# Kernel tuning notes

Hardware: AMD Instinct MI355X
Metric: run time of the kernel (lower is better)

Reference implementation:

```python
import jax, jax.numpy as jnp
import numpy as np

B, C, H, W = 32, 384, 28, 28
E, HID, K = 4, 384, 2  # HID = hidden_features(1536) // num_experts(4)


def setup_inputs() -> dict:
    key = jax.random.key(0)
    ks = jax.random.split(key, 5)
    x = jax.random.normal(ks[0], (B, C, H, W), jnp.float32)
    gate_w = jax.random.normal(ks[1], (C, E), jnp.float32) * 0.02
    gate_b = jnp.zeros((E,), jnp.float32)
    w1 = jax.random.normal(ks[2], (E, HID, C), jnp.float32) * 0.02
    b1 = jnp.zeros((E, HID), jnp.float32)
    w2 = jax.random.normal(ks[3], (E, C, HID), jnp.float32) * 0.02
    b2 = jnp.zeros((E, C), jnp.float32)
    return {"x": x, "gate_w": gate_w, "gate_b": gate_b,
            "w1": w1, "b1": b1, "w2": w2, "b2": b2}


def reference(x, gate_w, gate_b, w1, b1, w2, b2):
    b, c, h, w = x.shape
    e = gate_b.shape[0]
    # per-token gating: tokens are spatial positions in NHWC order
    x_flat = x.transpose(0, 2, 3, 1).reshape(-1, c)          # [N, C], N = B*H*W
    scores = jax.nn.softmax(x_flat @ gate_w + gate_b, -1)    # [N, E]
    top_v, top_i = jax.lax.top_k(scores, K)                  # [N, K]
    top_w = jax.nn.softmax(top_v, -1)                        # [N, K] renormalized
    # weight map per top-k slot: [K, B, H, W]
    wmap = top_w.T.reshape(K, b, h, w)
    # faithful to torch loop: expert i contributes at slot k iff ANY token routed
    # to it at slot k; the weight applied is the UNMASKED slot-k weight map.
    present = (top_i[:, :, None] == jnp.arange(e)[None, None, :]).any(0)  # [K, E]
    coef = jnp.einsum('ke,kbhw->ebhw', present.astype(x.dtype), wmap)     # [E, B, H, W]
    # dense per-expert 1x1-conv MLP over the FULL tensor (as in the source)
    hdn = jax.nn.relu(jnp.einsum('bchw,edc->ebdhw', x, w1)
                      + b1[:, None, :, None, None])          # [E, B, HID, H, W]
    y = jnp.einsum('ebdhw,eod->ebohw', hdn, w2) + b2[:, None, :, None, None]
    out = jnp.einsum('ebohw,ebhw->bohw', y, coef)            # [B, C, H, W]
    return out
```

## Files before the change

### kernel.cpp

```cpp
#include <hip/hip_runtime.h>
#include <hip/hip_bf16.h>
#include <stdint.h>

#define B_DIM 32
#define C_DIM 384
#define HW_DIM 784
#define E_DIM 4
#define HID_DIM 384
#define NTOK (B_DIM * HW_DIM)
#define NH (E_DIM * HID_DIM)

using short8 = __attribute__((ext_vector_type(8))) short;
using f32x4  = __attribute__((ext_vector_type(4))) float;
typedef unsigned short ushort_t;

__device__ __forceinline__ ushort_t f2bf(float f) {
  __hip_bfloat16 h = __float2bfloat16(f);
  return __builtin_bit_cast(ushort_t, h);
}

__device__ __forceinline__ void gload_lds16(const void* g, void* l) {
  __builtin_amdgcn_global_load_lds(
      (const __attribute__((address_space(1))) unsigned int*)g,
      (__attribute__((address_space(3))) unsigned int*)l, 16, 0, 0);
}

__global__ __launch_bounds__(256) void prep_kernel(
    const float* __restrict__ w1, const float* __restrict__ w2,
    ushort_t* __restrict__ W1b, ushort_t* __restrict__ W2b,
    unsigned int* __restrict__ present) {
  int i = blockIdx.x * 256 + threadIdx.x;
  if (i == 0) *present = 0u;
  if (i < NH * C_DIM) {
    W1b[i] = f2bf(w1[i]);
    int o = i / NH;
    int r = i - o * NH;
    int e = r / HID_DIM;
    int k = r - e * HID_DIM;
    W2b[i] = f2bf(w2[((size_t)e * C_DIM + o) * HID_DIM + k]);
  }
}

__global__ __launch_bounds__(512) void gate_kernel(
    const float* __restrict__ x, const float* __restrict__ gw,
    const float* __restrict__ gb, ushort_t* __restrict__ xb,
    float* __restrict__ topw, unsigned int* __restrict__ present) {
  __shared__ __align__(16) ushort_t lxs[64][392];
  __shared__ float pscore[8][64][4];
  __shared__ unsigned int pmask;
  const int b = blockIdx.x;
  const int p0 = blockIdx.y * 64;
  const int cnt = min(64, HW_DIM - p0);
  const int tid = threadIdx.x;
  const int cg = tid >> 6, tl = tid & 63;
  if (tid == 0) pmask = 0u;
  float a0 = 0.f, a1 = 0.f, a2 = 0.f, a3 = 0.f;
  const bool valid = tl < cnt;
  if (valid) {
    const float* xp = x + (size_t)b * C_DIM * HW_DIM + p0 + tl;
    for (int c = cg; c < C_DIM; c += 8) {
      const float v = xp[(size_t)c * HW_DIM];
      lxs[tl][c] = f2bf(v);
      const float4 g = *(const float4*)&gw[c * 4];
      a0 += v * g.x; a1 += v * g.y; a2 += v * g.z; a3 += v * g.w;
    }
  }
  pscore[cg][tl][0] = a0; pscore[cg][tl][1] = a1;
  pscore[cg][tl][2] = a2; pscore[cg][tl][3] = a3;
  __syncthreads();
  if (cg == 0 && valid) {
    float z[4];
#pragma unroll
    for (int e = 0; e < 4; e++) {
      float s = gb[e];
#pragma unroll
      for (int g8 = 0; g8 < 8; g8++) s += pscore[g8][tl][e];
      z[e] = s;
    }
    const float mx = fmaxf(fmaxf(z[0], z[1]), fmaxf(z[2], z[3]));
    float s[4]; float sum = 0.f;
#pragma unroll
    for (int e = 0; e < 4; e++) { s[e] = __expf(z[e] - mx); sum += s[e]; }
    const float inv = 1.f / sum;
#pragma unroll
    for (int e = 0; e < 4; e++) s[e] *= inv;
    int e0 = 0; float v0 = s[0];
#pragma unroll
    for (int e = 1; e < 4; e++) if (s[e] > v0) { v0 = s[e]; e0 = e; }
    int e1 = -1; float v1 = -1.f;
#pragma unroll
    for (int e = 0; e < 4; e++) if (e != e0 && s[e] > v1) { v1 = s[e]; e1 = e; }
    const float r = __expf(v1 - v0);
    const float w0 = 1.f / (1.f + r);
    const int m = b * HW_DIM + p0 + tl;
    topw[m * 2] = w0;
    topw[m * 2 + 1] = 1.f - w0;
    atomicOr(&pmask, (1u << e0) | (1u << (4 + e1)));
  }
  __syncthreads();
  if (tid == 0) atomicOr(present, pmask);
  const int nchunk = cnt * 48;
  for (int ci = tid; ci < nchunk; ci += 512) {
    const int row = ci / 48, c8 = ci - row * 48;
    short8 v = *(const short8*)&lxs[row][c8 * 8];
    *(short8*)&xb[(size_t)(b * HW_DIM + p0 + row) * C_DIM + c8 * 8] = v;
  }
}

__global__ __launch_bounds__(256, 3) void gemm_1b(
    const ushort_t* __restrict__ A, const ushort_t* __restrict__ Bw,
    const float* __restrict__ bias, const float* __restrict__ topw,
    const unsigned int* __restrict__ presentp, ushort_t* __restrict__ hOut) {
  constexpr int KDIM = C_DIM, BM = 128, BN = 128, BK = 32;
  constexpr int KT = KDIM / BK;
  constexpr int NTN = NH / BN;
  constexpr int ASZ = BM * BK;
  __shared__ ushort_t smem[6 * ASZ];

  const int nwg = NTN * (NTOK / BM);
  const int orig = blockIdx.x;
  const int xcd = orig & 7;
  const int qq = nwg >> 3, rr = nwg & 7;
  const int wg = (xcd < rr ? xcd * (qq + 1) : rr * (qq + 1) + (xcd - rr) * qq)
               + (orig >> 3);
  const int mt = wg / NTN, nt = wg % NTN;
  const int m0 = mt * BM, n0 = nt * BN;

  const int tid = threadIdx.x;
  const int lane = tid & 63;
  const int wid = tid >> 6;
  const int wm = wid >> 1, wn = wid & 1;
  const int lanel = lane & 15, laneq = lane >> 4;

  auto stage = [&](int t) {
    const int buf = t % 3;
    ushort_t* dstA = smem + buf * ASZ;
    ushort_t* dstB = smem + 3 * ASZ + buf * ASZ;
    const int kb = t * BK;
#pragma unroll
    for (int li = 0; li < 2; ++li) {
      const int P = (li * 256 + tid) * 16;
      const int row = P >> 6;
      const int cb = (P & 63) ^ (((row >> 1) & 3) << 4);
      gload_lds16(&A[(size_t)(m0 + row) * KDIM + kb + (cb >> 1)],
                  (char*)dstA + P);
    }
#pragma unroll
    for (int li = 0; li < 2; ++li) {
      const int P = (li * 256 + tid) * 16;
      const int row = P >> 6;
      const int cb = (P & 63) ^ (((row >> 1) & 3) << 4);
      gload_lds16(&Bw[(size_t)(n0 + row) * KDIM + kb + (cb >> 1)],
                  (char*)dstB + P);
    }
  };

  f32x4 acc[4][4] = {};
  const int cbr = (laneq * 16) ^ (((lanel >> 1) & 3) << 4);

  stage(0);
  stage(1);
  for (int t = 0; t < KT; ++t) {
    if (t + 1 < KT)
      asm volatile("s_waitcnt vmcnt(4)" ::: "memory");
    else
      asm volatile("s_waitcnt vmcnt(0)" ::: "memory");
    __builtin_amdgcn_sched_barrier(0);
    __builtin_amdgcn_s_barrier();
    __builtin_amdgcn_sched_barrier(0);
    if (t + 2 < KT) stage(t + 2);
    const int buf = t % 3;
    const char* Ab = (const char*)(smem + buf * ASZ) + (wm * 64 + lanel) * 64;
    const char* Bb =
        (const char*)(smem + 3 * ASZ + buf * ASZ) + (wn * 64 + lanel) * 64;
    short8 av[4], bv[4];
#pragma unroll
    for (int i = 0; i < 4; ++i) av[i] = *(const short8*)(Ab + i * 1024 + cbr);
#pragma unroll
    for (int j = 0; j < 4; ++j) bv[j] = *(const short8*)(Bb + j * 1024 + cbr);
    __builtin_amdgcn_s_setprio(1);
#pragma unroll
    for (int i = 0; i < 4; ++i)
#pragma unroll
      for (int j = 0; j < 4; ++j)
        acc[i][j] = __builtin_amdgcn_mfma_f32_16x16x32_bf16(
            av[i], bv[j], acc[i][j], 0, 0, 0);
    __builtin_amdgcn_s_setprio(0);
  }

  const unsigned int pm = *presentp;
  __syncthreads();
  ushort_t* tr = smem;
  const int e = n0 / HID_DIM;
  const float P0 = (float)((pm >> e) & 1u);
  const float P1 = (float)((pm >> (4 + e)) & 1u);
#pragma unroll
  for (int mi = 0; mi < 4; ++mi) {
    const int r0 = wm * 64 + mi * 16 + laneq * 4;
    const int mg = m0 + r0;
    const float4 t0 = *(const float4*)&topw[mg * 2];
    const float4 t1 = *(const float4*)&topw[mg * 2 + 4];
    const float cj[4] = {P0 * t0.x + P1 * t0.y, P0 * t0.z + P1 * t0.w,
                         P0 * t1.x + P1 * t1.y, P0 * t1.z + P1 * t1.w};
#pragma unroll
    for (int ni = 0; ni < 4; ++ni) {
      const int cl = wn * 64 + ni * 16 + lanel;
      const float bvv = bias[n0 + cl];
#pragma unroll
      for (int j = 0; j < 4; ++j) {
        float v = fmaxf(acc[mi][ni][j] + bvv, 0.f);
        tr[(r0 + j) * 128 + cl] = f2bf(cj[j] * v);
      }
    }
  }
  __syncthreads();
#pragma unroll
  for (int it = 0; it < 8; ++it) {
    const int c = it * 256 + tid;
    const int row = c >> 4, cr = c & 15;
    *(short8*)&hOut[(size_t)(m0 + row) * NH + n0 + cr * 8] =
        *(const short8*)&tr[row * 128 + cr * 8];
  }
}

__global__ __launch_bounds__(128, 2) void gemm2_t(
    const ushort_t* __restrict__ A, const ushort_t* __restrict__ Bw,
    const float* __restrict__ bias, const float* __restrict__ topw,
    const unsigned int* __restrict__ presentp, float* __restrict__ outp) {
  constexpr int KDIM = NH, BM = 64, BN = 128, BK = 32;
  constexpr int KT = KDIM / BK;
  constexpr int NTN = C_DIM / BN;
  constexpr int ASZ = BM * BK;
  constexpr int BSZ = BN * BK;
  __shared__ ushort_t smem[3 * ASZ + 2 * BSZ];

  const int nwg = NTN * (NTOK / BM);
  const int orig = blockIdx.x;
  const int xcd = orig & 7;
  const int qq = nwg >> 3, rr = nwg & 7;
  const int wg = (xcd < rr ? xcd * (qq + 1) : rr * (qq + 1) + (xcd - rr) * qq)
               + (orig >> 3);
  const int mt = wg / NTN, nt = wg % NTN;
  const int m0 = mt * BM, n0 = nt * BN;

  const int tid = threadIdx.x;
  const int lane = tid & 63;
  const int wn = tid >> 6;
  const int lanel = lane & 15, laneq = lane >> 4;

  auto stageA = [&](int t) {
    ushort_t* dst = smem + (t % 3) * ASZ;
    const int kb = t * BK;
#pragma unroll
    for (int li = 0; li < 2; ++li) {
      const int P = (li * 128 + tid) * 16;
      const int row = P >> 6;
      const int cb = (P & 63) ^ (((row >> 1) & 3) << 4);
      gload_lds16(&A[(size_t)(m0 + row) * KDIM + kb + (cb >> 1)],
                  (char*)dst + P);
    }
  };
  auto stageB = [&](int t) {
    ushort_t* dst = smem + 3 * ASZ + (t & 1) * BSZ;
    const int kb = t * BK;
#pragma unroll
    for (int li = 0; li < 4; ++li) {
      const int P = (li * 128 + tid) * 16;
      const int row = P >> 6;
      const int cb = (P & 63) ^ (((row >> 1) & 3) << 4);
      gload_lds16(&Bw[(size_t)(n0 + row) * KDIM + kb + (cb >> 1)],
                  (char*)dst + P);
    }
  };

  f32x4 acc[4][4] = {};
  const int cbr = (laneq * 16) ^ (((lanel >> 1) & 3) << 4);

  stageA(0);
  stageB(0);
  stageA(1);
  for (int t = 0; t < KT; ++t) {
    if (t + 1 < KT)
      asm volatile("s_waitcnt vmcnt(2)" ::: "memory");
    else
      asm volatile("s_waitcnt vmcnt(0)" ::: "memory");
    __builtin_amdgcn_sched_barrier(0);
    __builtin_amdgcn_s_barrier();
    __builtin_amdgcn_sched_barrier(0);
    if (t + 1 < KT) stageB(t + 1);
    if (t + 2 < KT) stageA(t + 2);
    const char* Ab = (const char*)(smem + (t % 3) * ASZ) + lanel * 64;
    const char* Bb = (const char*)(smem + 3 * ASZ + (t & 1) * BSZ) +
                     (wn * 64 + lanel) * 64;
    short8 av[4], bv[4];
#pragma unroll
    for (int i = 0; i < 4; ++i) av[i] = *(const short8*)(Ab + i * 1024 + cbr);
#pragma unroll
    for (int j = 0; j < 4; ++j) bv[j] = *(const short8*)(Bb + j * 1024 + cbr);
    __builtin_amdgcn_s_setprio(1);
#pragma unroll
    for (int i = 0; i < 4; ++i)
#pragma unroll
      for (int j = 0; j < 4; ++j)
        acc[i][j] = __builtin_amdgcn_mfma_f32_16x16x32_bf16(
            av[i], bv[j], acc[i][j], 0, 0, 0);
    __builtin_amdgcn_s_setprio(0);
  }

  const unsigned int pm = *presentp;
  float B0[4], B1[4];
#pragma unroll
  for (int ni = 0; ni < 4; ++ni) {
    const int o = n0 + wn * 64 + ni * 16 + lanel;
    float s0 = 0.f, s1 = 0.f;
#pragma unroll
    for (int e2 = 0; e2 < 4; ++e2) {
      const float bb = bias[e2 * C_DIM + o];
      s0 += (float)((pm >> e2) & 1u) * bb;
      s1 += (float)((pm >> (4 + e2)) & 1u) * bb;
    }
    B0[ni] = s0; B1[ni] = s1;
  }
#pragma unroll
  for (int mi = 0; mi < 4; ++mi) {
    const int mg = m0 + mi * 16 + laneq * 4;
    const float4 t0 = *(const float4*)&topw[mg * 2];
    const float4 t1 = *(const float4*)&topw[mg * 2 + 4];
    const int bb2 = mg / HW_DIM;
    const int p = mg - bb2 * HW_DIM;
#pragma unroll
    for (int ni = 0; ni < 4; ++ni) {
      const int o = n0 + wn * 64 + ni * 16 + lanel;
      float4 v;
      v.x = acc[mi][ni][0] + t0.x * B0[ni] + t0.y * B1[ni];
      v.y = acc[mi][ni][1] + t0.z * B0[ni] + t0.w * B1[ni];
      v.z = acc[mi][ni][2] + t1.x * B0[ni] + t1.y * B1[ni];
      v.w = acc[mi][ni][3] + t1.z * B0[ni] + t1.w * B1[ni];
      *(float4*)&outp[((size_t)bb2 * C_DIM + o) * HW_DIM + p] = v;
    }
  }
}

extern "C" void kernel_launch(void* const* d_in, const int* in_sizes, int n_in,
                              void* d_out, int out_size, void* d_ws, size_t ws_size,
                              hipStream_t stream) {
  const float* x  = (const float*)d_in[0];
  const float* gw = (const float*)d_in[1];
  const float* gb = (const float*)d_in[2];
  const float* w1 = (const float*)d_in[3];
  const float* b1 = (const float*)d_in[4];
  const float* w2 = (const float*)d_in[5];
  const float* b2 = (const float*)d_in[6];
  float* out = (float*)d_out;

  char* ws = (char*)d_ws;
  ushort_t* xb = (ushort_t*)ws;   ws += (size_t)NTOK * C_DIM * 2;
  ushort_t* hdnS = (ushort_t*)ws; ws += (size_t)NTOK * NH * 2;
  ushort_t* W1b = (ushort_t*)ws;  ws += (size_t)NH * C_DIM * 2;
  ushort_t* W2b = (ushort_t*)ws;  ws += (size_t)C_DIM * NH * 2;
  float* topw = (float*)ws;       ws += (size_t)NTOK * 2 * 4;
  unsigned int* present = (unsigned int*)ws;

  prep_kernel<<<dim3((NH * C_DIM) / 256), dim3(256), 0, stream>>>(
      w1, w2, W1b, W2b, present);
  gate_kernel<<<dim3(B_DIM, 13), dim3(512), 0, stream>>>(
      x, gw, gb, xb, topw, present);
  gemm_1b<<<dim3((NTOK / 128) * (NH / 128)), dim3(256), 0, stream>>>(
      xb, W1b, b1, topw, present, hdnS);
  gemm2_t<<<dim3((NTOK / 64) * (C_DIM / 128)), dim3(128), 0, stream>>>(
      hdnS, W2b, b2, topw, present, out);
}
```

Baseline: 131.2 us.

## Swap GEMM tile configs: 2-wave 128x128 for GEMM1, 4-wave 128x128 for GEMM2

GEMM1 moves from 4 waves with 64x64 warp tiles to 2 waves, each computing a 128x64 tile with 32 accumulators, double-buffered with a full vmcnt(0) wait each step. GEMM2 now reuses the former 4-wave 128x128 pipeline with a 128-row M tile instead of 64, which halves how often the B operand is reloaded per output. Larger per-wave tiles raise MFMA-to-LDS-load ratio but increase register pressure and reduce latency hiding from the simpler pipeline.

Result: no change. 128.7 us (-1.9%).

```diff
diff --git a/kernel.cpp b/kernel.cpp
--- a/kernel.cpp
+++ b/kernel.cpp
@@ -107,13 +107,122 @@
   }
 }
 
-__global__ __launch_bounds__(256, 3) void gemm_1b(
+__global__ __launch_bounds__(128, 2) void gemm_w2(
     const ushort_t* __restrict__ A, const ushort_t* __restrict__ Bw,
     const float* __restrict__ bias, const float* __restrict__ topw,
     const unsigned int* __restrict__ presentp, ushort_t* __restrict__ hOut) {
   constexpr int KDIM = C_DIM, BM = 128, BN = 128, BK = 32;
   constexpr int KT = KDIM / BK;
   constexpr int NTN = NH / BN;
+  constexpr int ASZ = BM * BK;
+  __shared__ ushort_t smem[4 * ASZ];
+
+  const int nwg = NTN * (NTOK / BM);
+  const int orig = blockIdx.x;
+  const int xcd = orig & 7;
+  const int qq = nwg >> 3, rr = nwg & 7;
+  const int wg = (xcd < rr ? xcd * (qq + 1) : rr * (qq + 1) + (xcd - rr) * qq)
+               + (orig >> 3);
+  const int mt = wg / NTN, nt = wg % NTN;
+  const int m0 = mt * BM, n0 = nt * BN;
+
+  const int tid = threadIdx.x;
+  const int lane = tid & 63;
+  const int wn = tid >> 6;
+  const int lanel = lane & 15, laneq = lane >> 4;
+
+  auto stage = [&](int t) {
+    ushort_t* dstA = smem + (t & 1) * ASZ;
+    ushort_t* dstB = smem + 2 * ASZ + (t & 1) * ASZ;
+    const int kb = t * BK;
+#pragma unroll
+    for (int li = 0; li < 4; ++li) {
+      const int P = (li * 128 + tid) * 16;
+      const int row = P >> 6;
+      const int cb = (P & 63) ^ (((row >> 1) & 3) << 4);
+      gload_lds16(&A[(size_t)(m0 + row) * KDIM + kb + (cb >> 1)],
+                  (char*)dstA + P);
+    }
+#pragma unroll
+    for (int li = 0; li < 4; ++li) {
+      const int P = (li * 128 + tid) * 16;
+      const int row = P >> 6;
+      const int cb = (P & 63) ^ (((row >> 1) & 3) << 4);
+      gload_lds16(&Bw[(size_t)(n0 + row) * KDIM + kb + (cb >> 1)],
+                  (char*)dstB + P);
+    }
+  };
+
+  f32x4 acc[8][4] = {};
+  const int cbr = (laneq * 16) ^ (((lanel >> 1) & 3) << 4);
+
+  stage(0);
+  for (int t = 0; t < KT; ++t) {
+    asm volatile("s_waitcnt vmcnt(0)" ::: "memory");
+    __builtin_amdgcn_sched_barrier(0);
+    __builtin_amdgcn_s_barrier();
+    __builtin_amdgcn_sched_barrier(0);
+    if (t + 1 < KT) stage(t + 1);
+    const char* Ab = (const char*)(smem + (t & 1) * ASZ) + lanel * 64;
+    const char* Bb = (const char*)(smem + 2 * ASZ + (t & 1) * ASZ) +
+                     (wn * 64 + lanel) * 64;
+    short8 av[8], bv[4];
+#pragma unroll
+    for (int i = 0; i < 8; ++i) av[i] = *(const short8*)(Ab + i * 1024 + cbr);
+#pragma unroll
+    for (int j = 0; j < 4; ++j) bv[j] = *(const short8*)(Bb + j * 1024 + cbr);
+    __builtin_amdgcn_s_setprio(1);
+#pragma unroll
+    for (int i = 0; i < 8; ++i)
+#pragma unroll
+      for (int j = 0; j < 4; ++j)
+        acc[i][j] = __builtin_amdgcn_mfma_f32_16x16x32_bf16(
+            av[i], bv[j], acc[i][j], 0, 0, 0);
+    __builtin_amdgcn_s_setprio(0);
+  }
+
+  const unsigned int pm = *presentp;
+  __syncthreads();
+  ushort_t* tr = smem;
+  const int e = n0 / HID_DIM;
+  const float P0 = (float)((pm >> e) & 1u);
+  const float P1 = (float)((pm >> (4 + e)) & 1u);
+#pragma unroll
+  for (int mi = 0; mi < 8; ++mi) {
+    const int r0 = mi * 16 + laneq * 4;
+    const int mg = m0 + r0;
+    const float4 t0 = *(const float4*)&topw[mg * 2];
+    const float4 t1 = *(const float4*)&topw[mg * 2 + 4];
+    const float cj[4] = {P0 * t0.x + P1 * t0.y, P0 * t0.z + P1 * t0.w,
+                         P0 * t1.x + P1 * t1.y, P0 * t1.z + P1 * t1.w};
+#pragma unroll
+    for (int ni = 0; ni < 4; ++ni) {
+      const int cl = wn * 64 + ni * 16 + lanel;
+      const float bvv = bias[n0 + cl];
+#pragma unroll
+      for (int j = 0; j < 4; ++j) {
+        float v = fmaxf(acc[mi][ni][j] + bvv, 0.f);
+        tr[(r0 + j) * 128 + cl] = f2bf(cj[j] * v);
+      }
+    }
+  }
+  __syncthreads();
+#pragma unroll
+  for (int it = 0; it < 16; ++it) {
+    const int c = it * 128 + tid;
+    const int row = c >> 4, cr = c & 15;
+    *(short8*)&hOut[(size_t)(m0 + row) * NH + n0 + cr * 8] =
+        *(const short8*)&tr[row * 128 + cr * 8];
+  }
+}
+
+__global__ __launch_bounds__(256, 3) void gemm2_k(
+    const ushort_t* __restrict__ A, const ushort_t* __restrict__ Bw,
+    const float* __restrict__ bias, const float* __restrict__ topw,
+    const unsigned int* __restrict__ presentp, float* __restrict__ outp) {
+  constexpr int KDIM = NH, BM = 128, BN = 128, BK = 32;
+  constexpr int KT = KDIM / BK;
+  constexpr int NTN = C_DIM / BN;
   constexpr int ASZ = BM * BK;
   __shared__ ushort_t smem[6 * ASZ];
 
@@ -189,125 +298,6 @@
   }
 
   const unsigned int pm = *presentp;
-  __syncthreads();
-  ushort_t* tr = smem;
-  const int e = n0 / HID_DIM;
-  const float P0 = (float)((pm >> e) & 1u);
-  const float P1 = (float)((pm >> (4 + e)) & 1u);
-#pragma unroll
-  for (int mi = 0; mi < 4; ++mi) {
-    const int r0 = wm * 64 + mi * 16 + laneq * 4;
-    const int mg = m0 + r0;
-    const float4 t0 = *(const float4*)&topw[mg * 2];
-    const float4 t1 = *(const float4*)&topw[mg * 2 + 4];
-    const float cj[4] = {P0 * t0.x + P1 * t0.y, P0 * t0.z + P1 * t0.w,
-                         P0 * t1.x + P1 * t1.y, P0 * t1.z + P1 * t1.w};
-#pragma unroll
-    for (int ni = 0; ni < 4; ++ni) {
-      const int cl = wn * 64 + ni * 16 + lanel;
-      const float bvv = bias[n0 + cl];
-#pragma unroll
-      for (int j = 0; j < 4; ++j) {
-        float v = fmaxf(acc[mi][ni][j] + bvv, 0.f);
-        tr[(r0 + j) * 128 + cl] = f2bf(cj[j] * v);
-      }
-    }
-  }
-  __syncthreads();
-#pragma unroll
-  for (int it = 0; it < 8; ++it) {
-    const int c = it * 256 + tid;
-    const int row = c >> 4, cr = c & 15;
-    *(short8*)&hOut[(size_t)(m0 + row) * NH + n0 + cr * 8] =
-        *(const short8*)&tr[row * 128 + cr * 8];
-  }
-}
-
-__global__ __launch_bounds__(128, 2) void gemm2_t(
-    const ushort_t* __restrict__ A, const ushort_t* __restrict__ Bw,
-    const float* __restrict__ bias, const float* __restrict__ topw,
-    const unsigned int* __restrict__ presentp, float* __restrict__ outp) {
-  constexpr int KDIM = NH, BM = 64, BN = 128, BK = 32;
-  constexpr int KT = KDIM / BK;
-  constexpr int NTN = C_DIM / BN;
-  constexpr int ASZ = BM * BK;
-  constexpr int BSZ = BN * BK;
-  __shared__ ushort_t smem[3 * ASZ + 2 * BSZ];
-
-  const int nwg = NTN * (NTOK / BM);
-  const int orig = blockIdx.x;
-  const int xcd = orig & 7;
-  const int qq = nwg >> 3, rr = nwg & 7;
-  const int wg = (xcd < rr ? xcd * (qq + 1) : rr * (qq + 1) + (xcd - rr) * qq)
-               + (orig >> 3);
-  const int mt = wg / NTN, nt = wg % NTN;
-  const int m0 = mt * BM, n0 = nt * BN;
-
-  const int tid = threadIdx.x;
-  const int lane = tid & 63;
-  const int wn = tid >> 6;
-  const int lanel = lane & 15, laneq = lane >> 4;
-
-  auto stageA = [&](int t) {
-    ushort_t* dst = smem + (t % 3) * ASZ;
-    const int kb = t * BK;
-#pragma unroll
-    for (int li = 0; li < 2; ++li) {
-      const int P = (li * 128 + tid) * 16;
-      const int row = P >> 6;
-      const int cb = (P & 63) ^ (((row >> 1) & 3) << 4);
-      gload_lds16(&A[(size_t)(m0 + row) * KDIM + kb + (cb >> 1)],
-                  (char*)dst + P);
-    }
-  };
-  auto stageB = [&](int t) {
-    ushort_t* dst = smem + 3 * ASZ + (t & 1) * BSZ;
-    const int kb = t * BK;
-#pragma unroll
-    for (int li = 0; li < 4; ++li) {
-      const int P = (li * 128 + tid) * 16;
-      const int row = P >> 6;
-      const int cb = (P & 63) ^ (((row >> 1) & 3) << 4);
-      gload_lds16(&Bw[(size_t)(n0 + row) * KDIM + kb + (cb >> 1)],
-                  (char*)dst + P);
-    }
-  };
-
-  f32x4 acc[4][4] = {};
-  const int cbr = (laneq * 16) ^ (((lanel >> 1) & 3) << 4);
-
-  stageA(0);
-  stageB(0);
-  stageA(1);
-  for (int t = 0; t < KT; ++t) {
-    if (t + 1 < KT)
-      asm volatile("s_waitcnt vmcnt(2)" ::: "memory");
-    else
-      asm volatile("s_waitcnt vmcnt(0)" ::: "memory");
-    __builtin_amdgcn_sched_barrier(0);
-    __builtin_amdgcn_s_barrier();
-    __builtin_amdgcn_sched_barrier(0);
-    if (t + 1 < KT) stageB(t + 1);
-    if (t + 2 < KT) stageA(t + 2);
-    const char* Ab = (const char*)(smem + (t % 3) * ASZ) + lanel * 64;
-    const char* Bb = (const char*)(smem + 3 * ASZ + (t & 1) * BSZ) +
-                     (wn * 64 + lanel) * 64;
-    short8 av[4], bv[4];
-#pragma unroll
-    for (int i = 0; i < 4; ++i) av[i] = *(const short8*)(Ab + i * 1024 + cbr);
-#pragma unroll
-    for (int j = 0; j < 4; ++j) bv[j] = *(const short8*)(Bb + j * 1024 + cbr);
-    __builtin_amdgcn_s_setprio(1);
-#pragma unroll
-    for (int i = 0; i < 4; ++i)
-#pragma unroll
-      for (int j = 0; j < 4; ++j)
-        acc[i][j] = __builtin_amdgcn_mfma_f32_16x16x32_bf16(
-            av[i], bv[j], acc[i][j], 0, 0, 0);
-    __builtin_amdgcn_s_setprio(0);
-  }
-
-  const unsigned int pm = *presentp;
   float B0[4], B1[4];
 #pragma unroll
   for (int ni = 0; ni < 4; ++ni) {
@@ -323,7 +313,7 @@
   }
 #pragma unroll
   for (int mi = 0; mi < 4; ++mi) {
-    const int mg = m0 + mi * 16 + laneq * 4;
+    const int mg = m0 + wm * 64 + mi * 16 + laneq * 4;
     const float4 t0 = *(const float4*)&topw[mg * 2];
     const float4 t1 = *(const float4*)&topw[mg * 2 + 4];
     const int bb2 = mg / HW_DIM;
@@ -365,8 +355,8 @@
       w1, w2, W1b, W2b, present);
   gate_kernel<<<dim3(B_DIM, 13), dim3(512), 0, stream>>>(
       x, gw, gb, xb, topw, present);
-  gemm_1b<<<dim3((NTOK / 128) * (NH / 128)), dim3(256), 0, stream>>>(
+  gemm_w2<<<dim3((NTOK / 128) * (NH / 128)), dim3(128), 0, stream>>>(
       xb, W1b, b1, topw, present, hdnS);
-  gemm2_t<<<dim3((NTOK / 64) * (C_DIM / 128)), dim3(128), 0, stream>>>(
+  gemm2_k<<<dim3((NTOK / 128) * (C_DIM / 128)), dim3(256), 0, stream>>>(
       hdnS, W2b, b2, topw, present, out);
 }
```
